# Optimization experiments

Measured on AMD Instinct MI355X. Metric: run time of the kernel, lower is better.

The kernel has to match this reference:

```python
import jax, jax.numpy as jnp
import numpy as np

NUM_CLASSES = 80
FOCAL_ALPHA = 0.25
FOCAL_GAMMA = 2.0
HUBER_SIGMA = 3.0
REG_MEAN = 0.0
REG_STD = 0.2
POS_THRESH = 0.5
NEG_THRESH = 0.4
EPS = 1e-4


def _iou(anchors, boxes):
    # anchors [A,4], boxes [M,4] -> [A,M]
    a = anchors[:, None, :]
    b = boxes[None, :, :]
    iw = jnp.clip(jnp.minimum(a[..., 2], b[..., 2]) - jnp.maximum(a[..., 0], b[..., 0]), 0.0)
    ih = jnp.clip(jnp.minimum(a[..., 3], b[..., 3]) - jnp.maximum(a[..., 1], b[..., 1]), 0.0)
    inter = iw * ih
    area_a = (a[..., 2] - a[..., 0]) * (a[..., 3] - a[..., 1])
    area_b = (b[..., 2] - b[..., 0]) * (b[..., 3] - b[..., 1])
    return inter / jnp.clip(area_a + area_b - inter, 1e-8)


def _bbox_transform(anchors, gt):
    # keras-retinanet style: per-coordinate offsets normalized by anchor w/h
    aw = anchors[:, 2] - anchors[:, 0]
    ah = anchors[:, 3] - anchors[:, 1]
    t = jnp.stack([(gt[:, 0] - anchors[:, 0]) / aw,
                   (gt[:, 1] - anchors[:, 1]) / ah,
                   (gt[:, 2] - anchors[:, 2]) / aw,
                   (gt[:, 3] - anchors[:, 3]) / ah], axis=1)
    return (t - REG_MEAN) / REG_STD


def _targets_one_image(anchor, ann, image_shape):
    # anchor [A,4], ann [M,5]
    iou = _iou(anchor, ann[:, :4])              # [A,M]
    best = jnp.argmax(iou, axis=1)              # [A]
    max_iou = jnp.max(iou, axis=1)
    pos = max_iou >= POS_THRESH
    ign = (max_iou > NEG_THRESH) & (~pos)
    states = jnp.where(pos, 1.0, jnp.where(ign, -1.0, 0.0))
    # ignore anchors whose center falls outside the image
    cx = (anchor[:, 0] + anchor[:, 2]) * 0.5
    cy = (anchor[:, 1] + anchor[:, 3]) * 0.5
    outside = (cx >= image_shape[1].astype(cx.dtype)) | (cy >= image_shape[0].astype(cy.dtype))
    states = jnp.where(outside, -1.0, states)
    assigned = ann[best]                        # [A,5]
    labels = jax.nn.one_hot(assigned[:, 4].astype(jnp.int32), NUM_CLASSES, dtype=anchor.dtype)
    labels = labels * pos[:, None].astype(anchor.dtype)
    regression = _bbox_transform(anchor, assigned[:, :4])
    return regression, labels, states


def setup_inputs() -> dict:
    key = jax.random.key(0)
    B, A, C, M = 8, 120000, NUM_CLASSES, 32
    k = jax.random.split(key, 10)
    # anchors: random centers/sizes inside an 800x800 image
    cx = jax.random.uniform(k[0], (B, A), minval=0.0, maxval=800.0)
    cy = jax.random.uniform(k[1], (B, A), minval=0.0, maxval=800.0)
    w = jax.random.uniform(k[2], (B, A), minval=16.0, maxval=256.0)
    h = jax.random.uniform(k[3], (B, A), minval=16.0, maxval=256.0)
    anchors = jnp.stack([cx - w / 2, cy - h / 2, cx + w / 2, cy + h / 2], axis=-1)
    # annotations: valid boxes (x1<x2, y1<y2) + class id
    x1 = jax.random.uniform(k[4], (B, M), minval=0.0, maxval=600.0)
    y1 = jax.random.uniform(k[5], (B, M), minval=0.0, maxval=600.0)
    bw = jax.random.uniform(k[6], (B, M), minval=32.0, maxval=180.0)
    bh = jax.random.uniform(k[7], (B, M), minval=32.0, maxval=180.0)
    cls = jax.random.randint(k[8], (B, M), 0, C).astype(jnp.float32)
    batch_annotations = jnp.stack([x1, y1, x1 + bw, y1 + bh, cls], axis=-1)
    # make sure positives exist: first M anchors per image ~= GT boxes (small jitter)
    jitter = 2.0 * jax.random.normal(k[9], (B, M, 4))
    anchors = anchors.at[:, :M, :].set(batch_annotations[:, :, :4] + jitter)
    output_classification = jax.random.uniform(jax.random.fold_in(key, 1), (B, A, C), minval=0.01, maxval=0.99)
    output_regression = jax.random.normal(jax.random.fold_in(key, 2), (B, A, 4))
    image_shape = jnp.array([800, 800], dtype=jnp.int32)
    return {"output_regression": output_regression,
            "output_classification": output_classification,
            "batch_annotations": batch_annotations,
            "anchors": anchors,
            "image_shape": image_shape}


def reference(output_regression, output_classification, batch_annotations, anchors, image_shape):
    reg_t, lab_t, states = jax.vmap(lambda a, an: _targets_one_image(a, an, image_shape))(
        anchors, batch_annotations)
    num_pos = jnp.sum((states == 1.0).astype(jnp.float32))
    normalizer = jnp.maximum(num_pos, 1.0)
    # focal loss (classification output already sigmoid probabilities)
    valid = (states != -1.0)[..., None].astype(output_classification.dtype)
    p = jnp.clip(output_classification, EPS, 1.0 - EPS)
    is_pos = lab_t == 1.0
    alpha_factor = jnp.where(is_pos, FOCAL_ALPHA, 1.0 - FOCAL_ALPHA)
    focal_weight = alpha_factor * jnp.where(is_pos, 1.0 - p, p) ** FOCAL_GAMMA
    bce = -(lab_t * jnp.log(p) + (1.0 - lab_t) * jnp.log1p(-p))
    cls_loss = jnp.sum(focal_weight * bce * valid) / normalizer
    # smooth L1 on positive anchors
    sigma_sq = HUBER_SIGMA ** 2
    diff = jnp.abs(output_regression - reg_t)
    sl1 = jnp.where(diff < 1.0 / sigma_sq, 0.5 * sigma_sq * diff * diff, diff - 0.5 / sigma_sq)
    pos_mask = (states == 1.0)[..., None].astype(output_regression.dtype)
    reg_loss = jnp.sum(sl1 * pos_mask) / normalizer
    return cls_loss + reg_loss
```

## Files before the change

### kernel.cpp

```cpp
#include <hip/hip_runtime.h>
#include <hip/hip_bf16.h>


#define CLS 80
#define F4_PER_ANCHOR (CLS / 4)
#define MAXM 32

#define META_BYTES   960000
#define NBLK_ANCHOR  3752
#define NBLK_CLS     4096

__global__ void anchor_kernel(const float* __restrict__ anchors,
                              const float* __restrict__ ann,
                              const float* __restrict__ out_reg,
                              const int*   __restrict__ image_shape,
                              unsigned char* __restrict__ meta,
                              float* __restrict__ reg_part,
                              float* __restrict__ cnt_part,
                              int A, int M) {
    __shared__ float s_ann[MAXM * 5];
    __shared__ float s_area[MAXM];
    __shared__ float s_red[4][2];
    const int b   = blockIdx.y;
    const int tid = threadIdx.x;
    const float* annb = ann + (size_t)b * M * 5;
    if (tid < M * 5) s_ann[tid] = annb[tid];
    __syncthreads();
    if (tid < M) {
        float x1 = s_ann[tid * 5 + 0], y1 = s_ann[tid * 5 + 1];
        float x2 = s_ann[tid * 5 + 2], y2 = s_ann[tid * 5 + 3];
        s_area[tid] = (x2 - x1) * (y2 - y1);
    }
    __syncthreads();

    const int a = blockIdx.x * blockDim.x + tid;
    float regv = 0.0f, cntv = 0.0f;

    if (a < A) {
        const size_t idx = (size_t)b * A + a;
        const float4 an = ((const float4*)anchors)[idx];
        const float area_a = (an.z - an.x) * (an.w - an.y);

        float maxiou = -1.0f;
        int best = 0;
        #pragma unroll
        for (int j = 0; j < MAXM; ++j) {
            const float bx1 = s_ann[j * 5 + 0], by1 = s_ann[j * 5 + 1];
            const float bx2 = s_ann[j * 5 + 2], by2 = s_ann[j * 5 + 3];
            float iw = fminf(an.z, bx2) - fmaxf(an.x, bx1);
            iw = fmaxf(iw, 0.0f);
            float ih = fminf(an.w, by2) - fmaxf(an.y, by1);
            ih = fmaxf(ih, 0.0f);
            const float inter = iw * ih;
            const float iou = inter / fmaxf(area_a + s_area[j] - inter, 1e-8f);
            if (iou > maxiou) { maxiou = iou; best = j; }
        }

        const bool pos = (maxiou >= 0.5f);
        const bool ign = (maxiou > 0.4f) && !pos;
        const float cx = (an.x + an.z) * 0.5f;
        const float cy = (an.y + an.w) * 0.5f;
        const bool outside = (cx >= (float)image_shape[1]) || (cy >= (float)image_shape[0]);

        int state = pos ? 1 : (ign ? -1 : 0);
        if (outside) state = -1;

        unsigned char m;
        if (state == -1)      m = 0xFF;
        else if (state == 1)  m = (unsigned char)(int)s_ann[best * 5 + 4];
        else                  m = 0x80;
        meta[idx] = m;

        if (state == 1) {
            const float aw = an.z - an.x;
            const float ah = an.w - an.y;
            float t0 = ((s_ann[best * 5 + 0] - an.x) / aw) * 5.0f;
            float t1 = ((s_ann[best * 5 + 1] - an.y) / ah) * 5.0f;
            float t2 = ((s_ann[best * 5 + 2] - an.z) / aw) * 5.0f;
            float t3 = ((s_ann[best * 5 + 3] - an.w) / ah) * 5.0f;
            const float4 r = ((const float4*)out_reg)[idx];
            const float d0 = fabsf(r.x - t0), d1 = fabsf(r.y - t1);
            const float d2 = fabsf(r.z - t2), d3 = fabsf(r.w - t3);
            float reg = 0.0f;
            reg += (d0 < (1.0f/9.0f)) ? (4.5f * d0 * d0) : (d0 - (0.5f/9.0f));
            reg += (d1 < (1.0f/9.0f)) ? (4.5f * d1 * d1) : (d1 - (0.5f/9.0f));
            reg += (d2 < (1.0f/9.0f)) ? (4.5f * d2 * d2) : (d2 - (0.5f/9.0f));
            reg += (d3 < (1.0f/9.0f)) ? (4.5f * d3 * d3) : (d3 - (0.5f/9.0f));
            regv = reg;
            cntv = 1.0f;
        }
    }

    #pragma unroll
    for (int off = 32; off > 0; off >>= 1) {
        regv += __shfl_down(regv, off, 64);
        cntv += __shfl_down(cntv, off, 64);
    }
    const int lane = tid & 63, wid = tid >> 6;
    if (lane == 0) { s_red[wid][0] = regv; s_red[wid][1] = cntv; }
    __syncthreads();
    if (tid == 0) {
        const int blk = blockIdx.y * gridDim.x + blockIdx.x;
        reg_part[blk] = s_red[0][0] + s_red[1][0] + s_red[2][0] + s_red[3][0];
        cnt_part[blk] = s_red[0][1] + s_red[1][1] + s_red[2][1] + s_red[3][1];
    }
}

__global__ void cls_kernel(const float* __restrict__ cls,
                           const unsigned char* __restrict__ meta,
                           float* __restrict__ cls_part,
                           int n4) {
    const int i0     = blockIdx.x * blockDim.x + threadIdx.x;
    const int stride = gridDim.x * blockDim.x;
    float partial = 0.0f;

    for (int i = i0; i < n4; i += stride) {
        const int anchor = i / F4_PER_ANCHOR;
        const unsigned char m = meta[anchor];
        if (m == 0xFF) continue;
        const float4 p4 = ((const float4*)cls)[i];
        const int c0 = (i - anchor * F4_PER_ANCHOR) * 4;
        const int lab = (m < 0x80) ? (int)m : -1;

        const float pv[4] = {p4.x, p4.y, p4.z, p4.w};
        #pragma unroll
        for (int k = 0; k < 4; ++k) {
            float p = fminf(fmaxf(pv[k], 1e-4f), 1.0f - 1e-4f);
            const bool is_pos = (lab == c0 + k);
            const float pt    = is_pos ? (1.0f - p) : p;
            const float alpha = is_pos ? 0.25f : 0.75f;
            partial += alpha * pt * pt * (-__logf(1.0f - pt));
        }
    }

    __shared__ float red[4];
    #pragma unroll
    for (int off = 32; off > 0; off >>= 1) partial += __shfl_down(partial, off, 64);
    const int lane = threadIdx.x & 63;
    const int wid  = threadIdx.x >> 6;
    if (lane == 0) red[wid] = partial;
    __syncthreads();
    if (threadIdx.x == 0)
        cls_part[blockIdx.x] = red[0] + red[1] + red[2] + red[3];
}

__global__ void final_kernel(const float* __restrict__ reg_part,
                             const float* __restrict__ cnt_part,
                             const float* __restrict__ cls_part,
                             int n_anchor_blk, int n_cls_blk,
                             float* __restrict__ out) {
    float r = 0.0f, c = 0.0f, cl = 0.0f;
    for (int i = threadIdx.x; i < n_anchor_blk; i += blockDim.x) {
        r += reg_part[i];
        c += cnt_part[i];
    }
    for (int i = threadIdx.x; i < n_cls_blk; i += blockDim.x)
        cl += cls_part[i];

    #pragma unroll
    for (int off = 32; off > 0; off >>= 1) {
        r  += __shfl_down(r,  off, 64);
        c  += __shfl_down(c,  off, 64);
        cl += __shfl_down(cl, off, 64);
    }
    __shared__ float red[16][3];
    const int lane = threadIdx.x & 63, wid = threadIdx.x >> 6;
    if (lane == 0) { red[wid][0] = r; red[wid][1] = c; red[wid][2] = cl; }
    __syncthreads();
    if (threadIdx.x == 0) {
        float rs = 0.0f, cs = 0.0f, cls = 0.0f;
        const int nw = blockDim.x >> 6;
        for (int w = 0; w < nw; ++w) { rs += red[w][0]; cs += red[w][1]; cls += red[w][2]; }
        out[0] = (cls + rs) / fmaxf(cs, 1.0f);
    }
}

extern "C" void kernel_launch(void* const* d_in, const int* in_sizes, int n_in,
                              void* d_out, int out_size, void* d_ws, size_t ws_size,
                              hipStream_t stream) {
    const float* out_reg = (const float*)d_in[0];
    const float* out_cls = (const float*)d_in[1];
    const float* ann     = (const float*)d_in[2];
    const float* anchors = (const float*)d_in[3];
    const int*   ishape  = (const int*)d_in[4];
    float* out = (float*)d_out;

    const int B  = in_sizes[2] / (MAXM * 5);
    const int BA = in_sizes[0] / 4;
    const int A  = BA / B;
    const int M  = MAXM;
    const int n4 = in_sizes[1] / 4;

    unsigned char* meta = (unsigned char*)d_ws;
    float* reg_part = (float*)((char*)d_ws + META_BYTES);
    float* cnt_part = (float*)((char*)d_ws + META_BYTES + 15008);
    float* cls_part = (float*)((char*)d_ws + META_BYTES + 30016);

    const int gx = (A + 255) / 256;
    dim3 g1(gx, B);
    anchor_kernel<<<g1, 256, 0, stream>>>(anchors, ann, out_reg, ishape, meta,
                                          reg_part, cnt_part, A, M);

    cls_kernel<<<NBLK_CLS, 256, 0, stream>>>(out_cls, meta, cls_part, n4);

    final_kernel<<<1, 1024, 0, stream>>>(reg_part, cnt_part, cls_part,
                                         gx * B, NBLK_CLS, out);
}
```

Baseline: 501.7 us.

## Fuse anchor assignment and focal-loss classification into one kernel

Merges the anchor-matching kernel and the classification focal-loss kernel into a single kernel: each block assigns its 256 anchors, keeps their state bytes in shared memory, then streams those anchors' class probabilities. This removes the global meta buffer round trip and one kernel launch. It also replaces the per-box IoU division with a cross-multiplied comparison and thresholds. The classification pass now runs over a fixed per-block slice rather than a grid-stride loop, which changes load balance and parallelism.

```diff
diff --git a/kernel.cpp b/kernel.cpp
--- a/kernel.cpp
+++ b/kernel.cpp
@@ -5,59 +5,59 @@
 #define CLS 80
 #define F4_PER_ANCHOR (CLS / 4)
 #define MAXM 32
+#define APB 256
 
-#define META_BYTES   960000
-#define NBLK_ANCHOR  3752
-#define NBLK_CLS     4096
-
-__global__ void anchor_kernel(const float* __restrict__ anchors,
-                              const float* __restrict__ ann,
-                              const float* __restrict__ out_reg,
-                              const int*   __restrict__ image_shape,
-                              unsigned char* __restrict__ meta,
-                              float* __restrict__ reg_part,
-                              float* __restrict__ cnt_part,
-                              int A, int M) {
+__global__ void __launch_bounds__(256)
+fused_kernel(const float* __restrict__ anchors,
+             const float* __restrict__ ann,
+             const float* __restrict__ out_reg,
+             const float* __restrict__ cls,
+             const int*   __restrict__ image_shape,
+             float* __restrict__ part,
+             int A) {
     __shared__ float s_ann[MAXM * 5];
     __shared__ float s_area[MAXM];
-    __shared__ float s_red[4][2];
+    __shared__ unsigned char s_meta[APB];
+    __shared__ float s_red[4][3];
+
     const int b   = blockIdx.y;
     const int tid = threadIdx.x;
-    const float* annb = ann + (size_t)b * M * 5;
-    if (tid < M * 5) s_ann[tid] = annb[tid];
+    const int a0  = blockIdx.x * APB;
+
+    const float* annb = ann + (size_t)b * MAXM * 5;
+    if (tid < MAXM * 5) s_ann[tid] = annb[tid];
     __syncthreads();
-    if (tid < M) {
-        float x1 = s_ann[tid * 5 + 0], y1 = s_ann[tid * 5 + 1];
-        float x2 = s_ann[tid * 5 + 2], y2 = s_ann[tid * 5 + 3];
+    if (tid < MAXM) {
+        const float x1 = s_ann[tid*5+0], y1 = s_ann[tid*5+1];
+        const float x2 = s_ann[tid*5+2], y2 = s_ann[tid*5+3];
         s_area[tid] = (x2 - x1) * (y2 - y1);
     }
     __syncthreads();
 
-    const int a = blockIdx.x * blockDim.x + tid;
     float regv = 0.0f, cntv = 0.0f;
-
+    const int a = a0 + tid;
     if (a < A) {
         const size_t idx = (size_t)b * A + a;
         const float4 an = ((const float4*)anchors)[idx];
         const float area_a = (an.z - an.x) * (an.w - an.y);
 
-        float maxiou = -1.0f;
+        float inter_b = 0.0f, union_b = 1.0f;
         int best = 0;
         #pragma unroll
         for (int j = 0; j < MAXM; ++j) {
-            const float bx1 = s_ann[j * 5 + 0], by1 = s_ann[j * 5 + 1];
-            const float bx2 = s_ann[j * 5 + 2], by2 = s_ann[j * 5 + 3];
-            float iw = fminf(an.z, bx2) - fmaxf(an.x, bx1);
-            iw = fmaxf(iw, 0.0f);
-            float ih = fminf(an.w, by2) - fmaxf(an.y, by1);
-            ih = fmaxf(ih, 0.0f);
+            const float bx1 = s_ann[j*5+0], by1 = s_ann[j*5+1];
+            const float bx2 = s_ann[j*5+2], by2 = s_ann[j*5+3];
+            const float iw = fmaxf(fminf(an.z, bx2) - fmaxf(an.x, bx1), 0.0f);
+            const float ih = fmaxf(fminf(an.w, by2) - fmaxf(an.y, by1), 0.0f);
             const float inter = iw * ih;
-            const float iou = inter / fmaxf(area_a + s_area[j] - inter, 1e-8f);
-            if (iou > maxiou) { maxiou = iou; best = j; }
+            const float uni = fmaxf(area_a + s_area[j] - inter, 1e-8f);
+            if (inter * union_b > inter_b * uni) {
+                inter_b = inter; union_b = uni; best = j;
+            }
         }
 
-        const bool pos = (maxiou >= 0.5f);
-        const bool ign = (maxiou > 0.4f) && !pos;
+        const bool pos = (2.0f * inter_b >= union_b);
+        const bool ign = (inter_b > 0.4f * union_b) && !pos;
         const float cx = (an.x + an.z) * 0.5f;
         const float cy = (an.y + an.w) * 0.5f;
         const bool outside = (cx >= (float)image_shape[1]) || (cy >= (float)image_shape[0]);
@@ -67,110 +67,97 @@
 
         unsigned char m;
         if (state == -1)      m = 0xFF;
-        else if (state == 1)  m = (unsigned char)(int)s_ann[best * 5 + 4];
+        else if (state == 1)  m = (unsigned char)(int)s_ann[best*5+4];
         else                  m = 0x80;
-        meta[idx] = m;
+        s_meta[tid] = m;
 
         if (state == 1) {
             const float aw = an.z - an.x;
             const float ah = an.w - an.y;
-            float t0 = ((s_ann[best * 5 + 0] - an.x) / aw) * 5.0f;
-            float t1 = ((s_ann[best * 5 + 1] - an.y) / ah) * 5.0f;
-            float t2 = ((s_ann[best * 5 + 2] - an.z) / aw) * 5.0f;
-            float t3 = ((s_ann[best * 5 + 3] - an.w) / ah) * 5.0f;
+            const float t0 = ((s_ann[best*5+0] - an.x) / aw) * 5.0f;
+            const float t1 = ((s_ann[best*5+1] - an.y) / ah) * 5.0f;
+            const float t2 = ((s_ann[best*5+2] - an.z) / aw) * 5.0f;
+            const float t3 = ((s_ann[best*5+3] - an.w) / ah) * 5.0f;
             const float4 r = ((const float4*)out_reg)[idx];
             const float d0 = fabsf(r.x - t0), d1 = fabsf(r.y - t1);
             const float d2 = fabsf(r.z - t2), d3 = fabsf(r.w - t3);
             float reg = 0.0f;
-            reg += (d0 < (1.0f/9.0f)) ? (4.5f * d0 * d0) : (d0 - (0.5f/9.0f));
-            reg += (d1 < (1.0f/9.0f)) ? (4.5f * d1 * d1) : (d1 - (0.5f/9.0f));
-            reg += (d2 < (1.0f/9.0f)) ? (4.5f * d2 * d2) : (d2 - (0.5f/9.0f));
-            reg += (d3 < (1.0f/9.0f)) ? (4.5f * d3 * d3) : (d3 - (0.5f/9.0f));
+            reg += (d0 < (1.0f/9.0f)) ? (4.5f*d0*d0) : (d0 - (0.5f/9.0f));
+            reg += (d1 < (1.0f/9.0f)) ? (4.5f*d1*d1) : (d1 - (0.5f/9.0f));
+            reg += (d2 < (1.0f/9.0f)) ? (4.5f*d2*d2) : (d2 - (0.5f/9.0f));
+            reg += (d3 < (1.0f/9.0f)) ? (4.5f*d3*d3) : (d3 - (0.5f/9.0f));
             regv = reg;
             cntv = 1.0f;
+        }
+    } else {
+        s_meta[tid] = 0xFF;
+    }
+    __syncthreads();
+
+    const int nA  = min(APB, A - a0);
+    const int nf4 = nA * F4_PER_ANCHOR;
+    const float4* cls4 = (const float4*)cls
+                       + ((size_t)b * A + a0) * F4_PER_ANCHOR;
+    float clsv = 0.0f;
+
+    for (int i = tid; i < nf4; i += APB) {
+        const int al = i / F4_PER_ANCHOR;
+        const unsigned char m = s_meta[al];
+        if (m == 0xFF) continue;
+        const float4 p4 = cls4[i];
+        const int c0  = (i - al * F4_PER_ANCHOR) * 4;
+        const int lab = (m < 0x80) ? (int)m : -1;
+
+        const float pv[4] = {p4.x, p4.y, p4.z, p4.w};
+        #pragma unroll
+        for (int k = 0; k < 4; ++k) {
+            const float p  = fminf(fmaxf(pv[k], 1e-4f), 1.0f - 1e-4f);
+            const bool is_pos = (lab == c0 + k);
+            const float pt    = is_pos ? (1.0f - p) : p;
+            const float alpha = is_pos ? 0.25f : 0.75f;
+            clsv += alpha * pt * pt * (-__logf(1.0f - pt));
         }
     }
 
     #pragma unroll
     for (int off = 32; off > 0; off >>= 1) {
+        clsv += __shfl_down(clsv, off, 64);
         regv += __shfl_down(regv, off, 64);
         cntv += __shfl_down(cntv, off, 64);
     }
     const int lane = tid & 63, wid = tid >> 6;
-    if (lane == 0) { s_red[wid][0] = regv; s_red[wid][1] = cntv; }
+    if (lane == 0) { s_red[wid][0] = clsv; s_red[wid][1] = regv; s_red[wid][2] = cntv; }
     __syncthreads();
     if (tid == 0) {
         const int blk = blockIdx.y * gridDim.x + blockIdx.x;
-        reg_part[blk] = s_red[0][0] + s_red[1][0] + s_red[2][0] + s_red[3][0];
-        cnt_part[blk] = s_red[0][1] + s_red[1][1] + s_red[2][1] + s_red[3][1];
+        part[blk*3+0] = s_red[0][0] + s_red[1][0] + s_red[2][0] + s_red[3][0];
+        part[blk*3+1] = s_red[0][1] + s_red[1][1] + s_red[2][1] + s_red[3][1];
+        part[blk*3+2] = s_red[0][2] + s_red[1][2] + s_red[2][2] + s_red[3][2];
     }
 }
 
-__global__ void cls_kernel(const float* __restrict__ cls,
-                           const unsigned char* __restrict__ meta,
-                           float* __restrict__ cls_part,
-                           int n4) {
-    const int i0     = blockIdx.x * blockDim.x + threadIdx.x;
-    const int stride = gridDim.x * blockDim.x;
-    float partial = 0.0f;
-
-    for (int i = i0; i < n4; i += stride) {
-        const int anchor = i / F4_PER_ANCHOR;
-        const unsigned char m = meta[anchor];
-        if (m == 0xFF) continue;
-        const float4 p4 = ((const float4*)cls)[i];
-        const int c0 = (i - anchor * F4_PER_ANCHOR) * 4;
-        const int lab = (m < 0x80) ? (int)m : -1;
-
-        const float pv[4] = {p4.x, p4.y, p4.z, p4.w};
-        #pragma unroll
-        for (int k = 0; k < 4; ++k) {
-            float p = fminf(fmaxf(pv[k], 1e-4f), 1.0f - 1e-4f);
-            const bool is_pos = (lab == c0 + k);
-            const float pt    = is_pos ? (1.0f - p) : p;
-            const float alpha = is_pos ? 0.25f : 0.75f;
-            partial += alpha * pt * pt * (-__logf(1.0f - pt));
-        }
+__global__ void final_kernel(const float* __restrict__ part, int n_blk,
+                             float* __restrict__ out) {
+    float cl = 0.0f, r = 0.0f, c = 0.0f;
+    for (int i = threadIdx.x; i < n_blk; i += blockDim.x) {
+        cl += part[i*3+0];
+        r  += part[i*3+1];
+        c  += part[i*3+2];
     }
-
-    __shared__ float red[4];
-    #pragma unroll
-    for (int off = 32; off > 0; off >>= 1) partial += __shfl_down(partial, off, 64);
-    const int lane = threadIdx.x & 63;
-    const int wid  = threadIdx.x >> 6;
-    if (lane == 0) red[wid] = partial;
-    __syncthreads();
-    if (threadIdx.x == 0)
-        cls_part[blockIdx.x] = red[0] + red[1] + red[2] + red[3];
-}
-
-__global__ void final_kernel(const float* __restrict__ reg_part,
-                             const float* __restrict__ cnt_part,
-                             const float* __restrict__ cls_part,
-                             int n_anchor_blk, int n_cls_blk,
-                             float* __restrict__ out) {
-    float r = 0.0f, c = 0.0f, cl = 0.0f;
-    for (int i = threadIdx.x; i < n_anchor_blk; i += blockDim.x) {
-        r += reg_part[i];
-        c += cnt_part[i];
-    }
-    for (int i = threadIdx.x; i < n_cls_blk; i += blockDim.x)
-        cl += cls_part[i];
-
     #pragma unroll
     for (int off = 32; off > 0; off >>= 1) {
+        cl += __shfl_down(cl, off, 64);
         r  += __shfl_down(r,  off, 64);
         c  += __shfl_down(c,  off, 64);
-        cl += __shfl_down(cl, off, 64);
     }
     __shared__ float red[16][3];
     const int lane = threadIdx.x & 63, wid = threadIdx.x >> 6;
-    if (lane == 0) { red[wid][0] = r; red[wid][1] = c; red[wid][2] = cl; }
+    if (lane == 0) { red[wid][0] = cl; red[wid][1] = r; red[wid][2] = c; }
     __syncthreads();
     if (threadIdx.x == 0) {
-        float rs = 0.0f, cs = 0.0f, cls = 0.0f;
+        float cls = 0.0f, rs = 0.0f, cs = 0.0f;
         const int nw = blockDim.x >> 6;
-        for (int w = 0; w < nw; ++w) { rs += red[w][0]; cs += red[w][1]; cls += red[w][2]; }
+        for (int w = 0; w < nw; ++w) { cls += red[w][0]; rs += red[w][1]; cs += red[w][2]; }
         out[0] = (cls + rs) / fmaxf(cs, 1.0f);
     }
 }
@@ -188,21 +175,13 @@
     const int B  = in_sizes[2] / (MAXM * 5);
     const int BA = in_sizes[0] / 4;
     const int A  = BA / B;
-    const int M  = MAXM;
-    const int n4 = in_sizes[1] / 4;
 
-    unsigned char* meta = (unsigned char*)d_ws;
-    float* reg_part = (float*)((char*)d_ws + META_BYTES);
-    float* cnt_part = (float*)((char*)d_ws + META_BYTES + 15008);
-    float* cls_part = (float*)((char*)d_ws + META_BYTES + 30016);
+    float* part = (float*)d_ws;
 
-    const int gx = (A + 255) / 256;
+    const int gx = (A + APB - 1) / APB;
     dim3 g1(gx, B);
-    anchor_kernel<<<g1, 256, 0, stream>>>(anchors, ann, out_reg, ishape, meta,
-                                          reg_part, cnt_part, A, M);
+    fused_kernel<<<g1, APB, 0, stream>>>(anchors, ann, out_reg, out_cls,
+                                         ishape, part, A);
 
-    cls_kernel<<<NBLK_CLS, 256, 0, stream>>>(out_cls, meta, cls_part, n4);
-
-    final_kernel<<<1, 1024, 0, stream>>>(reg_part, cnt_part, cls_part,
-                                         gx * B, NBLK_CLS, out);
+    final_kernel<<<1, 1024, 0, stream>>>(part, gx * B, out);
 }
```

Measured after the change: 490.9 us. 2.2% less time.
